# Kernel optimization log

Hardware: AMD Instinct MI355X
Metric: run time of the kernel (lower is better)

Reference implementation:

```python
import jax, jax.numpy as jnp
import numpy as np

B, N, E, P, PH, H = 4, 512, 768, 64, 32, 8
D = E // H  # 96
FFN = 3072

def _ln(x, g, b, eps=1e-5):
    mu = jnp.mean(x, axis=-1, keepdims=True)
    var = jnp.mean((x - mu) ** 2, axis=-1, keepdims=True)
    return (x - mu) * jax.lax.rsqrt(var + eps) * g + b

def setup_inputs() -> dict:
    key = jax.random.key(0)
    ks = iter(jax.random.split(key, 80))
    def f(*s):
        return jax.random.normal(next(ks), s, jnp.float32) * 0.02
    ones = lambda *s: jnp.ones(s, jnp.float32)
    zeros = lambda *s: jnp.zeros(s, jnp.float32)
    return {
        'x': jax.random.normal(next(ks), (B, N, E), jnp.float32),
        'pair': jax.random.normal(next(ks), (B, N, N, P), jnp.float32) * 0.5,
        'attn_mask': zeros(B, 1, N, N),
        'op_mask': ones(B, N, 1),
        'op_norm': ones(1) / N,
        'nlist': jax.random.randint(next(ks), (B, N, 64), 0, N),
        'wq': f(E, E), 'wk': f(E, E), 'wv': f(E, E),
        'wg': f(E, E), 'bg': zeros(E),
        'wo': f(E, E), 'bo': zeros(E),
        'ln_pair_g': ones(P), 'ln_pair_b': zeros(P),
        'wb': f(H, P), 'bb': zeros(H),
        'ln_attn_g': ones(E), 'ln_attn_b': zeros(E),
        'ln_ffn_g': ones(E), 'ln_ffn_b': zeros(E),
        'w_ffn1': f(FFN, E), 'b_ffn1': zeros(FFN),
        'w_ffn2': f(E, FFN), 'b_ffn2': zeros(E),
        'ln_opm_g': ones(E), 'ln_opm_b': zeros(E),
        'w_opm_in': f(2 * PH, E), 'b_opm_in': zeros(2 * PH),
        'w_opm_out': f(P, PH * PH), 'b_opm_out': zeros(P),
        'ln_tm_g': ones(P), 'ln_tm_b': zeros(P),
        'w_tm_abp': f(2 * PH, P), 'b_tm_abp': zeros(2 * PH),
        'w_tm_abg': f(2 * PH, P), 'b_tm_abg': zeros(2 * PH),
        'w_tm_g': f(P, P), 'b_tm_g': zeros(P),
        'w_tm_z': f(P, PH), 'b_tm_z': zeros(P),
        'ln_tmo_g': ones(PH), 'ln_tmo_b': zeros(PH),
        'ln_pffn_g': ones(P), 'ln_pffn_b': zeros(P),
        'w_pffn1': f(P, P), 'b_pffn1': zeros(P),
        'w_pffn2': f(P, P), 'b_pffn2': zeros(P),
    }

def _forward(x, pair, attn_mask, op_mask, op_norm, wq, wk, wv, wg, bg, wo, bo,
             ln_pair_g, ln_pair_b, wb, bb, ln_attn_g, ln_attn_b,
             ln_ffn_g, ln_ffn_b, w_ffn1, b_ffn1, w_ffn2, b_ffn2,
             ln_opm_g, ln_opm_b, w_opm_in, b_opm_in, w_opm_out, b_opm_out,
             ln_tm_g, ln_tm_b, w_tm_abp, b_tm_abp, w_tm_abg, b_tm_abg,
             w_tm_g, b_tm_g, w_tm_z, b_tm_z, ln_tmo_g, ln_tmo_b,
             ln_pffn_g, ln_pffn_b, w_pffn1, b_pffn1, w_pffn2, b_pffn2):
    Bx, Nx, _ = x.shape
    # --- gated pair-bias self-attention (pre-LN, eval mode: dropout = identity) ---
    h = _ln(x, ln_attn_g, ln_attn_b)
    pn = _ln(pair, ln_pair_g, ln_pair_b)               # AtomAttention pair LayerNorm
    bias = jnp.einsum('bijp,hp->bhij', pn, wb) + bb[None, :, None, None]
    q = (h @ wq.T).reshape(Bx, Nx, H, D).transpose(0, 2, 1, 3) * (D ** -0.5)
    k = (h @ wk.T).reshape(Bx, Nx, H, D).transpose(0, 2, 1, 3)
    v = (h @ wv.T).reshape(Bx, Nx, H, D).transpose(0, 2, 1, 3)
    attn = jax.nn.softmax(jnp.einsum('bhid,bhjd->bhij', q, k) + attn_mask + bias, axis=-1)
    o = jnp.einsum('bhij,bhjd->bhid', attn, v).transpose(0, 2, 1, 3).reshape(Bx, Nx, E)
    o = jax.nn.sigmoid(h @ wg.T + bg) * o              # sigmoid output gate
    x = x + (o @ wo.T + bo)
    # --- atom transition MLP ---
    h = _ln(x, ln_ffn_g, ln_ffn_b)
    x = x + (jax.nn.gelu(h @ w_ffn1.T + b_ffn1, approximate=False) @ w_ffn2.T + b_ffn2)
    # --- OuterProduct pair update (fused: avoids [B,N,N,PH*PH] intermediate) ---
    h = _ln(x, ln_opm_g, ln_opm_b)
    ab = (h @ w_opm_in.T + b_opm_in) * op_mask
    a_o, b_o = jnp.split(ab, 2, axis=-1)               # each [B,N,PH]
    z = jnp.einsum('bid,bje,pde->bijp', a_o, b_o, w_opm_out.reshape(P, PH, PH)) + b_opm_out
    pair = pair + z * op_norm
    # --- triangle multiplication ---
    zp = _ln(pair, ln_tm_g, ln_tm_b)
    gpr = zp @ w_tm_g.T + b_tm_g                       # gate (no sigmoid, matches source)
    ab = (zp @ w_tm_abp.T + b_tm_abp) * jax.nn.sigmoid(zp @ w_tm_abg.T + b_tm_abg)
    a_t, b_t = jnp.split(ab, 2, axis=-1)               # each [B,N,N,PH]
    t = jnp.einsum('bijh,bkjh->bhik', a_t, b_t) + jnp.einsum('bjih,bjkh->bhik', a_t, b_t)
    t = _ln(t.transpose(0, 2, 3, 1), ln_tmo_g, ln_tmo_b) @ w_tm_z.T + b_tm_z
    pair = pair + gpr * t
    # --- pair transition MLP ---
    zp = _ln(pair, ln_pffn_g, ln_pffn_b)
    pair = pair + (jax.nn.gelu(zp @ w_pffn1.T + b_pffn1, approximate=False) @ w_pffn2.T + b_pffn2)
    return x, pair

def reference(x, pair, attn_mask, op_mask, op_norm, nlist, wq, wk, wv, wg, bg, wo, bo,
              ln_pair_g, ln_pair_b, wb, bb, ln_attn_g, ln_attn_b,
              ln_ffn_g, ln_ffn_b, w_ffn1, b_ffn1, w_ffn2, b_ffn2,
              ln_opm_g, ln_opm_b, w_opm_in, b_opm_in, w_opm_out, b_opm_out,
              ln_tm_g, ln_tm_b, w_tm_abp, b_tm_abp, w_tm_abg, b_tm_abg,
              w_tm_g, b_tm_g, w_tm_z, b_tm_z, ln_tmo_g, ln_tmo_b,
              ln_pffn_g, ln_pffn_b, w_pffn1, b_pffn1, w_pffn2, b_pffn2):
    del nlist  # accepted by the torch module but unused in the math
    return _forward(x, pair, attn_mask, op_mask, op_norm, wq, wk, wv, wg, bg, wo, bo,
                    ln_pair_g, ln_pair_b, wb, bb, ln_attn_g, ln_attn_b,
                    ln_ffn_g, ln_ffn_b, w_ffn1, b_ffn1, w_ffn2, b_ffn2,
                    ln_opm_g, ln_opm_b, w_opm_in, b_opm_in, w_opm_out, b_opm_out,
                    ln_tm_g, ln_tm_b, w_tm_abp, b_tm_abp, w_tm_abg, b_tm_abg,
                    w_tm_g, b_tm_g, w_tm_z, b_tm_z, ln_tmo_g, ln_tmo_b,
                    ln_pffn_g, ln_pffn_b, w_pffn1, b_pffn1, w_pffn2, b_pffn2)
```

## Files before the change

### kernel.cpp

```cpp
#include <hip/hip_runtime.h>
#include <hip/hip_bf16.h>
#include <math.h>

#define Nn 512
#define Ee 768
#define Pp 64
#define PHh 32
#define Hh 8
#define Dd 96
#define NNe 262144
#define LNEPS 1e-5f

typedef __attribute__((ext_vector_type(8))) short bf8;
typedef __attribute__((ext_vector_type(4))) short bf4;
typedef __attribute__((ext_vector_type(4))) float f32x4;
#define MFMA(a,b,c) __builtin_amdgcn_mfma_f32_16x16x32_bf16(a,b,c,0,0,0)

__device__ __forceinline__ short f2bf(float f) {
  unsigned u = __builtin_bit_cast(unsigned, f);
  unsigned r = (u + 0x7fffu + ((u >> 16) & 1u)) >> 16;
  return (short)r;
}
__device__ __forceinline__ float bf2f(short s) {
  unsigned u = ((unsigned)(unsigned short)s) << 16;
// ... 244 lines not shown
        *(const bf8*)(A + (long)(m0 + r4 + 64) * 768 + k0 + c8);
    *(bf8*)&Bs[r4 * 40 + c8] = *(const bf8*)(W + (long)(n0 + r4) * 768 + k0 + c8);
    *(bf8*)&Bs[(r4 + 64) * 40 + c8] =
        *(const bf8*)(W + (long)(n0 + r4 + 64) * 768 + k0 + c8);
    __syncthreads();
    bf8 af[4], bfm[4];
#pragma unroll
    for (int mi = 0; mi < 4; ++mi)
      af[mi] = *(const bf8*)&As[(wr * 64 + mi * 16 + llo) * 40 + lhi * 8];
#pragma unroll
    for (int ni = 0; ni < 4; ++ni)
      bfm[ni] = *(const bf8*)&Bs[(wc * 64 + ni * 16 + llo) * 40 + lhi * 8];
#pragma unroll
    for (int mi = 0; mi < 4; ++mi)
#pragma unroll
      for (int ni = 0; ni < 4; ++ni)
        acc[mi][ni] = MFMA(af[mi], bfm[ni], acc[mi][ni]);
    __syncthreads();
  }
#pragma unroll
  for (int mi = 0; mi < 4; ++mi) {
    int gmb = m0 + wr * 64 + mi * 16 + lhi * 4;
#pragma unroll
    for (int ni = 0; ni < 4; ++ni) {
      int gn = n0 + wc * 64 + ni * 16 + llo;
      float bv = bias[gn];
#pragma unroll
      for (int r = 0; r < 4; ++r)
        outB[(long)(gmb + r) * 3072 + gn] = f2bf(gelu_exact(acc[mi][ni][r] + bv));
    }
  }
}

__global__ __launch_bounds__(256) void attn_fused(
    const short* __restrict__ q_bf, const short* __restrict__ k_bf,
    const short* __restrict__ bias_bf, const float* __restrict__ mask,
    short* __restrict__ out_bf) {
  int it = blockIdx.x, h = blockIdx.y, b = blockIdx.z;
  int tid = threadIdx.x;
  int wv = tid >> 6, lane = tid & 63;
  int lhi = lane >> 4, llo = lane & 15;
  int i0 = it * 16;
  long qoff = ((long)(b * 512 + i0)) * 768 + h * 96;
  bf8 qf[3];
#pragma unroll
  for (int ks = 0; ks < 3; ++ks)
    qf[ks] = *(const bf8*)(q_bf + qoff + (long)llo * 768 + ks * 32 + lhi * 8);
  long koff = ((long)b * 512) * 768 + h * 96;
  long bioff = (long)(b * 8 + h) * NNe + (long)i0 * 512;
  long moff = (long)b * NNe + (long)i0 * 512;
  float sv[8][4];
  int jb0 = wv * 128;
#pragma unroll
  for (int jf = 0; jf < 8; ++jf) {
    int jb = jb0 + jf * 16;
    f32x4 acc = {0.f, 0.f, 0.f, 0.f};
#pragma unroll
    for (int ks = 0; ks < 3; ++ks) {
      bf8 kf = *(const bf8*)(k_bf + koff + (long)(jb + llo) * 768 + ks * 32 + lhi * 8);
      acc = MFMA(qf[ks], kf, acc);
    }
#pragma unroll
    for (int r = 0; r < 4; ++r) {
      int irow = lhi * 4 + r;
      int j = jb + llo;
      float bia = bf2f(bias_bf[bioff + (long)irow * 512 + j]);
// ... 116 lines not shown
    }
    *(bf4*)&Zb[e * 72 + q * 16 + k * 4] = pk;
  }
  __syncthreads();
  int wv = tid >> 6, lane = tid & 63;
  int lhi = lane >> 4, llo = lane & 15;
  int n0 = wv * 16;
  f32x4 acc = {0.f, 0.f, 0.f, 0.f};
#pragma unroll
  for (int ks = 0; ks < 2; ++ks) {
    bf8 a = *(const bf8*)&Wb[llo * 72 + ks * 32 + lhi * 8];
    bf8 bz = *(const bf8*)&Zb[(n0 + llo) * 72 + ks * 32 + lhi * 8];
    acc = MFMA(a, bz, acc);
  }
  int elem = n0 + llo;
#pragma unroll
  for (int r = 0; r < 4; ++r) {
    int h = lhi * 4 + r;
    if (h < 8) bias[(long)(b * 8 + h) * NNe + ein + elem] = f2bf(acc[r] + bbv[h]);
  }
}

__global__ __launch_bounds__(256) void opm_ab_fused(
    const float* __restrict__ pair_in, const short* __restrict__ Tb,
    const short* __restrict__ bo_bf, const float* __restrict__ b_out,
    const float* __restrict__ op_norm, const float* __restrict__ gam,
    const float* __restrict__ bet, const short* __restrict__ wp_a,
    const float* __restrict__ b_abp, const short* __restrict__ wg_a,
    const float* __restrict__ b_abg,
    short* __restrict__ aN, short* __restrict__ bN) {
  int jt = blockIdx.x;
  int i = blockIdx.y;
  int tid = threadIdx.x;
  __shared__ __align__(16) short Tsb[64 * 40];
  __shared__ __align__(16) short Bob[64 * 40];
  __shared__ __align__(16) short Zb[64 * 72];
  __shared__ __align__(16) short Wp[64 * 72];
  __shared__ __align__(16) short Wg[64 * 72];
  __shared__ float spS[64][9];
  __shared__ float spQ[64][9];
  int wv = tid >> 6, lane = tid & 63;
  int wr = wv >> 1, wc = wv & 1;
  int lhi = lane >> 4, llo = lane & 15;
  int chb = wr * 32 + lhi * 4;
  {
    int p = tid >> 2, e8 = (tid & 3) * 8;
    *(bf8*)&Tsb[p * 40 + e8] = *(const bf8*)(Tb + (long)i * 2048 + p * 32 + e8);
    *(bf8*)&Bob[p * 40 + e8] = *(const bf8*)(bo_bf + (long)(jt * 64 + p) * 32 + e8);
  }
  for (int l = tid; l < 512; l += 256) {
    int r = l >> 3, c8 = (l & 7) * 8;
    *(bf8*)&Wp[r * 72 + c8] = *(const bf8*)(wp_a + r * 64 + c8);
    *(bf8*)&Wg[r * 72 + c8] = *(const bf8*)(wg_a + r * 64 + c8);
  }
  long ebase = (long)i * 512 + jt * 64;
  const float* pbase = pair_in + ebase * 64;
  f32x4 x[2][2];
#pragma unroll
  for (int mi = 0; mi < 2; ++mi)
#pragma unroll
    for (int ni = 0; ni < 2; ++ni)
      x[mi][ni] = *(const f32x4*)(pbase + (long)(wc * 32 + ni * 16 + llo) * 64 +
                                  chb + mi * 16);
  __syncthreads();
  f32x4 acc[2][2] = {};
  {
    bf8 a0 = *(const bf8*)&Tsb[(wr * 32 + llo) * 40 + lhi * 8];
    bf8 a1 = *(const bf8*)&Tsb[(wr * 32 + 16 + llo) * 40 + lhi * 8];
    bf8 b0 = *(const bf8*)&Bob[(wc * 32 + llo) * 40 + lhi * 8];
    bf8 b1 = *(const bf8*)&Bob[(wc * 32 + 16 + llo) * 40 + lhi * 8];
    acc[0][0] = MFMA(a0, b0, acc[0][0]);
    acc[0][1] = MFMA(a0, b1, acc[0][1]);
    acc[1][0] = MFMA(a1, b0, acc[1][0]);
    acc[1][1] = MFMA(a1, b1, acc[1][1]);
  }
  float nrm = op_norm[0];
#pragma unroll
  for (int mi = 0; mi < 2; ++mi) {
    f32x4 bo4 = *(const f32x4*)(b_out + chb + mi * 16);
#pragma unroll
    for (int ni = 0; ni < 2; ++ni)
#pragma unroll
      for (int r = 0; r < 4; ++r)
        x[mi][ni][r] += (acc[mi][ni][r] + bo4[r]) * nrm;
  }
#pragma unroll
  for (int ni = 0; ni < 2; ++ni) {
    float s = 0.f, ss = 0.f;
#pragma unroll
    for (int mi = 0; mi < 2; ++mi)
#pragma unroll
      for (int r = 0; r < 4; ++r) { float v = x[mi][ni][r]; s += v; ss += v * v; }
    int e = wc * 32 + ni * 16 + llo;
    spS[e][wr * 4 + lhi] = s;
    spQ[e][wr * 4 + lhi] = ss;
  }
  __syncthreads();
  float mu1[2], rs1[2];
#pragma unroll
  for (int ni = 0; ni < 2; ++ni) {
    int e = wc * 32 + ni * 16 + llo;
    float s = 0.f, q2 = 0.f;
#pragma unroll
    for (int k = 0; k < 8; ++k) { s += spS[e][k]; q2 += spQ[e][k]; }
    float mu = s * 0.015625f, var = q2 * 0.015625f - mu * mu;
    mu1[ni] = mu; rs1[ni] = rsqrtf(var + LNEPS);
  }
#pragma unroll
  for (int mi = 0; mi < 2; ++mi) {
    f32x4 gv = *(const f32x4*)(gam + chb + mi * 16);
    f32x4 bv = *(const f32x4*)(bet + chb + mi * 16);
#pragma unroll
    for (int ni = 0; ni < 2; ++ni) {
      int e = wc * 32 + ni * 16 + llo;
      bf4 pk;
#pragma unroll
      for (int r = 0; r < 4; ++r)
        pk[r] = f2bf((x[mi][ni][r] - mu1[ni]) * rs1[ni] * gv[r] + bv[r]);
      *(bf4*)&Zb[e * 72 + chb + mi * 16] = pk;
    }
  }
  __syncthreads();
  f32x4 ap[2][2] = {};
  f32x4 ag[2][2] = {};
#pragma unroll
  for (int ks = 0; ks < 2; ++ks) {
    bf8 z0 = *(const bf8*)&Zb[(wr * 32 + llo) * 72 + ks * 32 + lhi * 8];
    bf8 z1 = *(const bf8*)&Zb[(wr * 32 + 16 + llo) * 72 + ks * 32 + lhi * 8];
    bf8 p0 = *(const bf8*)&Wp[(wc * 32 + llo) * 72 + ks * 32 + lhi * 8];
    bf8 p1 = *(const bf8*)&Wp[(wc * 32 + 16 + llo) * 72 + ks * 32 + lhi * 8];
    bf8 g0 = *(const bf8*)&Wg[(wc * 32 + llo) * 72 + ks * 32 + lhi * 8];
    bf8 g1 = *(const bf8*)&Wg[(wc * 32 + 16 + llo) * 72 + ks * 32 + lhi * 8];
    ap[0][0] = MFMA(z0, p0, ap[0][0]);
    ap[0][1] = MFMA(z0, p1, ap[0][1]);
    ap[1][0] = MFMA(z1, p0, ap[1][0]);
    ap[1][1] = MFMA(z1, p1, ap[1][1]);
    ag[0][0] = MFMA(z0, g0, ag[0][0]);
    ag[0][1] = MFMA(z0, g1, ag[0][1]);
    ag[1][0] = MFMA(z1, g0, ag[1][0]);
    ag[1][1] = MFMA(z1, g1, ag[1][1]);
  }
#pragma unroll
  for (int mi = 0; mi < 2; ++mi) {
    int elemb = wr * 32 + mi * 16 + lhi * 4;
#pragma unroll
    for (int ni = 0; ni < 2; ++ni) {
      int ch = wc * 32 + ni * 16 + llo;
      float bp = b_abp[ch], bg = b_abg[ch];
      bf4 pack;
#pragma unroll
      for (int r = 0; r < 4; ++r)
        pack[r] = f2bf((ap[mi][ni][r] + bp) * sigmoidf_(ag[mi][ni][r] + bg));
      short* dst = (ch < 32) ? (aN + (long)ch * NNe) : (bN + (long)(ch - 32) * NNe);
      *(bf4*)(dst + ebase + elemb) = pack;
    }
  }
}

__global__ __launch_bounds__(512) void tm_tri_mfma(const short* __restrict__ aN,
                                                   const short* __restrict__ bN,
                                                   short* __restrict__ t_out) {
  int lin = blockIdx.z * 16 + blockIdx.y * 4 + blockIdx.x;
  int vid = (lin & 7) * 64 + (lin >> 3);
  int h = vid >> 4;
  int rem = vid & 15;
// ... 45 lines not shown
      bf8 c = *(const bf8*)&A2[(wr * 64 + mi * 16 + llo) * 40 + lhi * 8];
      acc[mi][0] = MFMA(c, dfr[0], acc[mi][0]);
      acc[mi][1] = MFMA(c, dfr[1], acc[mi][1]);
    }
    __syncthreads();
  }
  short* tp = t_out + (long)h * NNe;
#pragma unroll
  for (int mi = 0; mi < 4; ++mi)
#pragma unroll
    for (int ni = 0; ni < 2; ++ni) {
      int row = i0 + wr * 64 + mi * 16 + lhi * 4;
      int col = k0 + wc * 32 + ni * 16 + llo;
#pragma unroll
      for (int r = 0; r < 4; ++r) tp[(long)(row + r) * 512 + col] = f2bf(acc[mi][ni][r]);
    }
}

__global__ __launch_bounds__(256) void upd_pffn_fused(
    const float* __restrict__ pin, float* __restrict__ pout,
    const short* __restrict__ t_in,
    const short* __restrict__ Tb, const short* __restrict__ bo_bf,
    const float* __restrict__ b_out, const float* __restrict__ op_norm,
    const float* __restrict__ g_tm, const float* __restrict__ b_tm,
    const short* __restrict__ wg_a, const float* __restrict__ b_g,
    const short* __restrict__ wz_a, const float* __restrict__ b_z,
    const float* __restrict__ g_tmo, const float* __restrict__ b_tmo,
    const float* __restrict__ g_pf, const float* __restrict__ b_pf,
    const short* __restrict__ w1_a, const float* __restrict__ b1,
    const short* __restrict__ w2_a, const float* __restrict__ b2) {
  __shared__ __align__(16) short Zb[64 * 72];
  __shared__ __align__(16) short Tlb[64 * 40];
  __shared__ __align__(16) short Wbuf[64 * 72];
  __shared__ __align__(16) short Wzb[64 * 40];
  __shared__ __align__(16) short Tsb[64 * 40];
  __shared__ __align__(16) short Bob[64 * 40];
  __shared__ float spS[64][9];
  __shared__ float spQ[64][9];
  __shared__ float spB[4][2][72];
  int tid = threadIdx.x;
  long e0 = (long)blockIdx.x * 64;
  int i = (int)(e0 >> 9);
  int jt = (int)((e0 >> 6) & 7);
  int wv = tid >> 6, lane = tid & 63;
  int wr = wv >> 1, wc = wv & 1;
  int lhi = lane >> 4, llo = lane & 15;
  int chb = wr * 32 + lhi * 4;
  int r0 = tid >> 3, c0 = (tid & 7) * 8;
  int r1 = (tid + 256) >> 3, c1 = ((tid + 256) & 7) * 8;
  bf8 w1r0, w1r1, w2r0, w2r1;
  {
    *(bf8*)&Wbuf[r0 * 72 + c0] = *(const bf8*)(wg_a + r0 * 64 + c0);
    *(bf8*)&Wbuf[r1 * 72 + c1] = *(const bf8*)(wg_a + r1 * 64 + c1);
    w1r0 = *(const bf8*)(w1_a + r0 * 64 + c0);
    w1r1 = *(const bf8*)(w1_a + r1 * 64 + c1);
    w2r0 = *(const bf8*)(w2_a + r0 * 64 + c0);
    w2r1 = *(const bf8*)(w2_a + r1 * 64 + c1);
    int rz = tid >> 2, cz = (tid & 3) * 8;
    *(bf8*)&Wzb[rz * 40 + cz] = *(const bf8*)(wz_a + rz * 32 + cz);
    int p = tid >> 2, e8 = (tid & 3) * 8;
    *(bf8*)&Tsb[p * 40 + e8] = *(const bf8*)(Tb + (long)i * 2048 + p * 32 + e8);
    *(bf8*)&Bob[p * 40 + e8] = *(const bf8*)(bo_bf + (long)(jt * 64 + p) * 32 + e8);
  }
  f32x4 x[2][2];
#pragma unroll
  for (int mi = 0; mi < 2; ++mi)
#pragma unroll
    for (int ni = 0; ni < 2; ++ni)
      x[mi][ni] = *(const f32x4*)(pin + (e0 + wc * 32 + ni * 16 + llo) * 64 +
                                  chb + mi * 16);
  int te = tid & 63, tq = tid >> 6;
  float tt[8];
  {
    float sB = 0.f, ssB = 0.f;
#pragma unroll
    for (int k = 0; k < 8; ++k) {
      float v = bf2f(t_in[(long)(tq * 8 + k) * NNe + e0 + te]);
      tt[k] = v; sB += v; ssB += v * v;
    }
    spB[tq][0][te] = sB; spB[tq][1][te] = ssB;
  }
  __syncthreads();
  {
    float ts = spB[0][0][te] + spB[1][0][te] + spB[2][0][te] + spB[3][0][te];
    float tss = spB[0][1][te] + spB[1][1][te] + spB[2][1][te] + spB[3][1][te];
    float mu = ts * 0.03125f, var = tss * 0.03125f - mu * mu;
    float rs = rsqrtf(var + LNEPS);
    bf8 pk;
#pragma unroll
    for (int k = 0; k < 8; ++k) {
      int c = tq * 8 + k;
      pk[k] = f2bf((tt[k] - mu) * rs * g_tmo[c] + b_tmo[c]);
    }
    *(bf8*)&Tlb[te * 40 + tq * 8] = pk;
  }
  {
    f32x4 acc[2][2] = {};
    bf8 a0 = *(const bf8*)&Tsb[(wr * 32 + llo) * 40 + lhi * 8];
    bf8 a1 = *(const bf8*)&Tsb[(wr * 32 + 16 + llo) * 40 + lhi * 8];
    bf8 b0 = *(const bf8*)&Bob[(wc * 32 + llo) * 40 + lhi * 8];
    bf8 b1 = *(const bf8*)&Bob[(wc * 32 + 16 + llo) * 40 + lhi * 8];
    acc[0][0] = MFMA(a0, b0, acc[0][0]);
    acc[0][1] = MFMA(a0, b1, acc[0][1]);
    acc[1][0] = MFMA(a1, b0, acc[1][0]);
    acc[1][1] = MFMA(a1, b1, acc[1][1]);
    float nrm = op_norm[0];
#pragma unroll
    for (int mi = 0; mi < 2; ++mi) {
      f32x4 bo4 = *(const f32x4*)(b_out + chb + mi * 16);
#pragma unroll
      for (int ni = 0; ni < 2; ++ni)
#pragma unroll
        for (int r = 0; r < 4; ++r)
          x[mi][ni][r] += (acc[mi][ni][r] + bo4[r]) * nrm;
    }
  }
#pragma unroll
  for (int ni = 0; ni < 2; ++ni) {
    float s = 0.f, ss = 0.f;
#pragma unroll
    for (int mi = 0; mi < 2; ++mi)
#pragma unroll
      for (int r = 0; r < 4; ++r) { float v = x[mi][ni][r]; s += v; ss += v * v; }
    int e = wc * 32 + ni * 16 + llo;
    spS[e][wr * 4 + lhi] = s;
    spQ[e][wr * 4 + lhi] = ss;
  }
  __syncthreads();
  float mu1[2], rs1[2];
#pragma unroll
  for (int ni = 0; ni < 2; ++ni) {
    int e = wc * 32 + ni * 16 + llo;
    float s = 0.f, q2 = 0.f;
#pragma unroll
    for (int k = 0; k < 8; ++k) { s += spS[e][k]; q2 += spQ[e][k]; }
    float mu = s * 0.015625f, var = q2 * 0.015625f - mu * mu;
    mu1[ni] = mu; rs1[ni] = rsqrtf(var + LNEPS);
  }
#pragma unroll
  for (int mi = 0; mi < 2; ++mi) {
    f32x4 gv = *(const f32x4*)(g_tm + chb + mi * 16);
    f32x4 bv = *(const f32x4*)(b_tm + chb + mi * 16);
#pragma unroll
    for (int ni = 0; ni < 2; ++ni) {
      int e = wc * 32 + ni * 16 + llo;
      bf4 pk;
#pragma unroll
      for (int r = 0; r < 4; ++r)
        pk[r] = f2bf((x[mi][ni][r] - mu1[ni]) * rs1[ni] * gv[r] + bv[r]);
      *(bf4*)&Zb[e * 72 + chb + mi * 16] = pk;
    }
  }
  __syncthreads();
  f32x4 accg[2][2] = {};
  f32x4 accz[2][2] = {};
#pragma unroll
  for (int ks = 0; ks < 2; ++ks) {
    bf8 a0 = *(const bf8*)&Wbuf[(wr * 32 + llo) * 72 + ks * 32 + lhi * 8];
    bf8 a1 = *(const bf8*)&Wbuf[(wr * 32 + 16 + llo) * 72 + ks * 32 + lhi * 8];
    bf8 z0 = *(const bf8*)&Zb[(wc * 32 + llo) * 72 + ks * 32 + lhi * 8];
    bf8 z1 = *(const bf8*)&Zb[(wc * 32 + 16 + llo) * 72 + ks * 32 + lhi * 8];
    accg[0][0] = MFMA(a0, z0, accg[0][0]);
    accg[0][1] = MFMA(a0, z1, accg[0][1]);
    accg[1][0] = MFMA(a1, z0, accg[1][0]);
    accg[1][1] = MFMA(a1, z1, accg[1][1]);
  }
  {
    bf8 a0 = *(const bf8*)&Wzb[(wr * 32 + llo) * 40 + lhi * 8];
    bf8 a1 = *(const bf8*)&Wzb[(wr * 32 + 16 + llo) * 40 + lhi * 8];
    bf8 t0 = *(const bf8*)&Tlb[(wc * 32 + llo) * 40 + lhi * 8];
    bf8 t1 = *(const bf8*)&Tlb[(wc * 32 + 16 + llo) * 40 + lhi * 8];
    accz[0][0] = MFMA(a0, t0, accz[0][0]);
    accz[0][1] = MFMA(a0, t1, accz[0][1]);
    accz[1][0] = MFMA(a1, t0, accz[1][0]);
    accz[1][1] = MFMA(a1, t1, accz[1][1]);
  }
#pragma unroll
  for (int mi = 0; mi < 2; ++mi) {
    f32x4 bgv = *(const f32x4*)(b_g + chb + mi * 16);
    f32x4 bzv = *(const f32x4*)(b_z + chb + mi * 16);
#pragma unroll
    for (int ni = 0; ni < 2; ++ni)
#pragma unroll
      for (int r = 0; r < 4; ++r)
        x[mi][ni][r] += (accg[mi][ni][r] + bgv[r]) * (accz[mi][ni][r] + bzv[r]);
  }
#pragma unroll
  for (int ni = 0; ni < 2; ++ni) {
    float s = 0.f, ss = 0.f;
#pragma unroll
    for (int mi = 0; mi < 2; ++mi)
#pragma unroll
      for (int r = 0; r < 4; ++r) { float v = x[mi][ni][r]; s += v; ss += v * v; }
    int e = wc * 32 + ni * 16 + llo;
    spS[e][wr * 4 + lhi] = s;
    spQ[e][wr * 4 + lhi] = ss;
  }
  __syncthreads();
  *(bf8*)&Wbuf[r0 * 72 + c0] = w1r0;
  *(bf8*)&Wbuf[r1 * 72 + c1] = w1r1;
#pragma unroll
  for (int ni = 0; ni < 2; ++ni) {
    int e = wc * 32 + ni * 16 + llo;
    float s = 0.f, q2 = 0.f;
#pragma unroll
    for (int k = 0; k < 8; ++k) { s += spS[e][k]; q2 += spQ[e][k]; }
    float mu = s * 0.015625f, var = q2 * 0.015625f - mu * mu;
    mu1[ni] = mu; rs1[ni] = rsqrtf(var + LNEPS);
  }
#pragma unroll
  for (int mi = 0; mi < 2; ++mi) {
    f32x4 gv = *(const f32x4*)(g_pf + chb + mi * 16);
    f32x4 bv = *(const f32x4*)(b_pf + chb + mi * 16);
#pragma unroll
    for (int ni = 0; ni < 2; ++ni) {
      int e = wc * 32 + ni * 16 + llo;
      bf4 pk;
#pragma unroll
      for (int r = 0; r < 4; ++r)
        pk[r] = f2bf((x[mi][ni][r] - mu1[ni]) * rs1[ni] * gv[r] + bv[r]);
      *(bf4*)&Zb[e * 72 + chb + mi * 16] = pk;
    }
  }
  __syncthreads();
  f32x4 acc1[2][2] = {};
#pragma unroll
  for (int ks = 0; ks < 2; ++ks) {
    bf8 a0 = *(const bf8*)&Wbuf[(wr * 32 + llo) * 72 + ks * 32 + lhi * 8];
    bf8 a1 = *(const bf8*)&Wbuf[(wr * 32 + 16 + llo) * 72 + ks * 32 + lhi * 8];
    bf8 z0 = *(const bf8*)&Zb[(wc * 32 + llo) * 72 + ks * 32 + lhi * 8];
    bf8 z1 = *(const bf8*)&Zb[(wc * 32 + 16 + llo) * 72 + ks * 32 + lhi * 8];
    acc1[0][0] = MFMA(a0, z0, acc1[0][0]);
    acc1[0][1] = MFMA(a0, z1, acc1[0][1]);
    acc1[1][0] = MFMA(a1, z0, acc1[1][0]);
    acc1[1][1] = MFMA(a1, z1, acc1[1][1]);
  }
  __syncthreads();
  *(bf8*)&Wbuf[r0 * 72 + c0] = w2r0;
  *(bf8*)&Wbuf[r1 * 72 + c1] = w2r1;
#pragma unroll
  for (int mi = 0; mi < 2; ++mi) {
    f32x4 bv = *(const f32x4*)(b1 + chb + mi * 16);
#pragma unroll
    for (int ni = 0; ni < 2; ++ni) {
      int e = wc * 32 + ni * 16 + llo;
      bf4 pk;
#pragma unroll
      for (int r = 0; r < 4; ++r) pk[r] = f2bf(gelu_exact(acc1[mi][ni][r] + bv[r]));
      *(bf4*)&Zb[e * 72 + chb + mi * 16] = pk;
    }
  }
  __syncthreads();
  f32x4 acc2[2][2] = {};
#pragma unroll
  for (int ks = 0; ks < 2; ++ks) {
    bf8 a0 = *(const bf8*)&Wbuf[(wr * 32 + llo) * 72 + ks * 32 + lhi * 8];
    bf8 a1 = *(const bf8*)&Wbuf[(wr * 32 + 16 + llo) * 72 + ks * 32 + lhi * 8];
    bf8 z0 = *(const bf8*)&Zb[(wc * 32 + llo) * 72 + ks * 32 + lhi * 8];
    bf8 z1 = *(const bf8*)&Zb[(wc * 32 + 16 + llo) * 72 + ks * 32 + lhi * 8];
    acc2[0][0] = MFMA(a0, z0, acc2[0][0]);
    acc2[0][1] = MFMA(a0, z1, acc2[0][1]);
    acc2[1][0] = MFMA(a1, z0, acc2[1][0]);
    acc2[1][1] = MFMA(a1, z1, acc2[1][1]);
  }
#pragma unroll
  for (int mi = 0; mi < 2; ++mi) {
    f32x4 bv = *(const f32x4*)(b2 + chb + mi * 16);
#pragma unroll
    for (int ni = 0; ni < 2; ++ni) {
#pragma unroll
      for (int r = 0; r < 4; ++r) x[mi][ni][r] += acc2[mi][ni][r] + bv[r];
      *(f32x4*)(pout + (e0 + wc * 32 + ni * 16 + llo) * 64 + chb + mi * 16) =
          x[mi][ni];
    }
  }
}

extern "C" void kernel_launch(void* const* d_in, const int* in_sizes, int n_in,
                              void* d_out, int out_size, void* d_ws, size_t ws_size,
                              hipStream_t stream) {
  const float* x = (const float*)d_in[0];
  const float* pair = (const float*)d_in[1];
  const float* attn_mask = (const float*)d_in[2];
  const float* op_mask = (const float*)d_in[3];
  const float* op_norm = (const float*)d_in[4];
  const float* wq = (const float*)d_in[6];
  const float* wk = (const float*)d_in[7];
  const float* wv_ = (const float*)d_in[8];
  const float* wg = (const float*)d_in[9];
  const float* bg = (const float*)d_in[10];
  const float* wo = (const float*)d_in[11];
  const float* bo = (const float*)d_in[12];
// ... 54 lines not shown
  short* k_bf = (short*)(ws + 5442816);
  short* vT_bf = (short*)(ws + 6229248);
  float* gb = ws + 7015680;
  short* gb_bf = (short*)(ws + 10161408);
  float* x1b = ws + 10947840;
  short* biasb_bf = (short*)(ws + 12520704);
  short* attn_bf = (short*)(ws + 16715008);
  short* mffn_bf = (short*)(ws + 20909312);
  float* abb = ws + 24055040;
  short* abb_bf = (short*)(ws + 24186112);
  short* Tb_bf = (short*)(ws + 24218880);
  short* aNb = (short*)(ws + 4656384);
  short* bNb = (short*)(ws + 8850688);
  short* t_bf = (short*)(ws + 13044992);

  float* xo = (float*)d_out;
  float* pair1 = xo + 1572864;

  const float qscale = 0.1020620726159658f;

  castw_kernel<<<30144, 256, 0, stream>>>(wq, wk, wv_, wg, wo, w_ffn1, w_ffn2, w_opm_in,
                                          wbf, qscale);
  castw2_kernel<<<90, 256, 0, stream>>>(wb, w_tm_abp, w_tm_abg, w_tm_g, w_tm_z,
                                        w_pffn1, w_pffn2, wb_a);
  ln_bf_kernel<<<2048, 256, 0, stream>>>(x, h_bf, ln_attn_g, ln_attn_b, 768);
  gemm_qkvg<<<dim3(24, 16, 1), 256, 0, stream>>>(h_bf, wq_bf, q_bf, k_bf, vT_bf, gb, bg);
  pair_bias_mfma<<<16384, 256, 0, stream>>>(pair, ln_pair_g, ln_pair_b, wb_a, bb, biasb_bf);
  attn_fused<<<dim3(32, 8, 4), 256, 0, stream>>>(q_bf, k_bf, biasb_bf, attn_mask, attn_bf);
  gemm_bf<<<dim3(2, 8, 32), 256, 0, stream>>>(attn_bf, 512, 2097152, 262144,
                                              vT_bf, 512, 393216, 49152,
                                              nullptr, 0, 393216, 96, gb_bf, 768,
                                              gb, 768, 393216, 96, nullptr,
                                              512, 96, 512, 2, 0, 8);
  gemm_bf<<<dim3(12, 32, 1), 256, 0, stream>>>(gb_bf, 768, 0, 0, wo_bf, 768, 0, 0,
                                               x1b, 768, 0, 0, nullptr, 0,
                                               x, 768, 0, 0, bo,
                                               2048, 768, 768, 0, 0, 1);
  ln_bf_kernel<<<2048, 256, 0, stream>>>(x1b, h_bf, ln_ffn_g, ln_ffn_b, 768);
  gemm_ffn1<<<dim3(24, 16, 1), 256, 0, stream>>>(h_bf, wf1_bf, mffn_bf, b_ffn1);
  gemm_bf<<<dim3(12, 32, 1), 256, 0, stream>>>(mffn_bf, 3072, 0, 0, wf2_bf, 3072, 0, 0,
                                               xo, 768, 0, 0, nullptr, 0,
                                               x1b, 768, 0, 0, b_ffn2,
                                               2048, 768, 3072, 0, 0, 1);
  ln_bf_kernel<<<2048, 256, 0, stream>>>(xo, h_bf, ln_opm_g, ln_opm_b, 768);
  gemm_bf<<<dim3(1, 32, 1), 256, 0, stream>>>(h_bf, 768, 0, 0, wop_bf, 768, 0, 0,
                                              abb, 64, 0, 0, nullptr, 0,
                                              nullptr, 0, 0, 0, b_opm_in,
                                              2048, 64, 768, 0, 0, 1);
  opmask_kernel<<<512, 256, 0, stream>>>(abb, op_mask, abb_bf);
  opm_T_kernel<<<dim3(256, 64, 1), dim3(32, 8, 1), 0, stream>>>(abb, w_opm_out, Tb_bf);
  for (int b = 0; b < 4; ++b) {
    const float* pin = pair + (long)b * NNe * 64;
    float* pbb = pair1 + (long)b * NNe * 64;
    opm_ab_fused<<<dim3(8, 512, 1), 256, 0, stream>>>(
        pin, Tb_bf + (long)b * 1048576, abb_bf + (long)b * 16384, b_opm_out, op_norm,
        ln_tm_g, ln_tm_b, wabp_a, b_tm_abp, wabg_a, b_tm_abg, aNb, bNb);
    tm_tri_mfma<<<dim3(4, 4, 32), 512, 0, stream>>>(aNb, bNb, t_bf);
    upd_pffn_fused<<<4096, 256, 0, stream>>>(
        pin, pbb, t_bf, Tb_bf + (long)b * 1048576, abb_bf + (long)b * 16384,
        b_opm_out, op_norm,
        ln_tm_g, ln_tm_b, wtg_a, b_tm_g, wtz_a, b_tm_z,
        ln_tmo_g, ln_tmo_b, ln_pffn_g, ln_pffn_b, wp1_a, b_pffn1, wp2_a, b_pffn2);
  }
}
```

Before: 907.0 us.

## Use 128x128 GEMM for out-proj/FFN2 and load OPM fragments directly from global

```diff
diff --git a/kernel.cpp b/kernel.cpp
--- a/kernel.cpp
+++ b/kernel.cpp
@@ -300,6 +300,56 @@
   }
 }
 
+__global__ __launch_bounds__(256) void gemm128(
+    const short* __restrict__ A, const short* __restrict__ W, int K,
+    const float* __restrict__ resid, const float* __restrict__ bias,
+    float* __restrict__ outF) {
+  __shared__ __align__(16) short As[128 * 40];
+  __shared__ __align__(16) short Bs[128 * 40];
+  int m0 = blockIdx.y * 128, n0 = blockIdx.x * 128;
+  int tid = threadIdx.x;
+  int wv = tid >> 6, lane = tid & 63;
+  int wr = wv >> 1, wc = wv & 1;
+  int lhi = lane >> 4, llo = lane & 15;
+  int r4 = tid >> 2, c8 = (tid & 3) * 8;
+  f32x4 acc[4][4] = {};
+  for (int k0 = 0; k0 < K; k0 += 32) {
+    *(bf8*)&As[r4 * 40 + c8] = *(const bf8*)(A + (long)(m0 + r4) * K + k0 + c8);
+    *(bf8*)&As[(r4 + 64) * 40 + c8] =
+        *(const bf8*)(A + (long)(m0 + r4 + 64) * K + k0 + c8);
+    *(bf8*)&Bs[r4 * 40 + c8] = *(const bf8*)(W + (long)(n0 + r4) * K + k0 + c8);
+    *(bf8*)&Bs[(r4 + 64) * 40 + c8] =
+        *(const bf8*)(W + (long)(n0 + r4 + 64) * K + k0 + c8);
+    __syncthreads();
+    bf8 af[4], bfm[4];
+#pragma unroll
+    for (int mi = 0; mi < 4; ++mi)
+      af[mi] = *(const bf8*)&As[(wr * 64 + mi * 16 + llo) * 40 + lhi * 8];
+#pragma unroll
+    for (int ni = 0; ni < 4; ++ni)
+      bfm[ni] = *(const bf8*)&Bs[(wc * 64 + ni * 16 + llo) * 40 + lhi * 8];
+#pragma unroll
+    for (int mi = 0; mi < 4; ++mi)
+#pragma unroll
+      for (int ni = 0; ni < 4; ++ni)
+        acc[mi][ni] = MFMA(af[mi], bfm[ni], acc[mi][ni]);
+    __syncthreads();
+  }
+#pragma unroll
+  for (int mi = 0; mi < 4; ++mi) {
+    int gmb = m0 + wr * 64 + mi * 16 + lhi * 4;
+#pragma unroll
+    for (int ni = 0; ni < 4; ++ni) {
+      int gn = n0 + wc * 64 + ni * 16 + llo;
+      float bv = bias[gn];
+#pragma unroll
+      for (int r = 0; r < 4; ++r)
+        outF[(long)(gmb + r) * 768 + gn] =
+            acc[mi][ni][r] + bv + resid[(long)(gmb + r) * 768 + gn];
+    }
+  }
+}
+
 __global__ __launch_bounds__(256) void attn_fused(
     const short* __restrict__ q_bf, const short* __restrict__ k_bf,
     const short* __restrict__ bias_bf, const float* __restrict__ mask,
@@ -482,8 +532,6 @@
   int jt = blockIdx.x;
   int i = blockIdx.y;
   int tid = threadIdx.x;
-  __shared__ __align__(16) short Tsb[64 * 40];
-  __shared__ __align__(16) short Bob[64 * 40];
   __shared__ __align__(16) short Zb[64 * 72];
   __shared__ __align__(16) short Wp[64 * 72];
   __shared__ __align__(16) short Wg[64 * 72];
@@ -493,11 +541,7 @@
   int wr = wv >> 1, wc = wv & 1;
   int lhi = lane >> 4, llo = lane & 15;
   int chb = wr * 32 + lhi * 4;
-  {
-    int p = tid >> 2, e8 = (tid & 3) * 8;
-    *(bf8*)&Tsb[p * 40 + e8] = *(const bf8*)(Tb + (long)i * 2048 + p * 32 + e8);
-    *(bf8*)&Bob[p * 40 + e8] = *(const bf8*)(bo_bf + (long)(jt * 64 + p) * 32 + e8);
-  }
+  int fc = lhi * 8;
   for (int l = tid; l < 512; l += 256) {
     int r = l >> 3, c8 = (l & 7) * 8;
     *(bf8*)&Wp[r * 72 + c8] = *(const bf8*)(wp_a + r * 64 + c8);
@@ -512,27 +556,26 @@
     for (int ni = 0; ni < 2; ++ni)
       x[mi][ni] = *(const f32x4*)(pbase + (long)(wc * 32 + ni * 16 + llo) * 64 +
                                   chb + mi * 16);
-  __syncthreads();
-  f32x4 acc[2][2] = {};
   {
-    bf8 a0 = *(const bf8*)&Tsb[(wr * 32 + llo) * 40 + lhi * 8];
-    bf8 a1 = *(const bf8*)&Tsb[(wr * 32 + 16 + llo) * 40 + lhi * 8];
-    bf8 b0 = *(const bf8*)&Bob[(wc * 32 + llo) * 40 + lhi * 8];
-    bf8 b1 = *(const bf8*)&Bob[(wc * 32 + 16 + llo) * 40 + lhi * 8];
+    f32x4 acc[2][2] = {};
+    bf8 a0 = *(const bf8*)(Tb + (long)i * 2048 + (long)(wr * 32 + llo) * 32 + fc);
+    bf8 a1 = *(const bf8*)(Tb + (long)i * 2048 + (long)(wr * 32 + 16 + llo) * 32 + fc);
+    bf8 b0 = *(const bf8*)(bo_bf + (long)(jt * 64 + wc * 32 + llo) * 32 + fc);
+    bf8 b1 = *(const bf8*)(bo_bf + (long)(jt * 64 + wc * 32 + 16 + llo) * 32 + fc);
     acc[0][0] = MFMA(a0, b0, acc[0][0]);
     acc[0][1] = MFMA(a0, b1, acc[0][1]);
     acc[1][0] = MFMA(a1, b0, acc[1][0]);
     acc[1][1] = MFMA(a1, b1, acc[1][1]);
-  }
-  float nrm = op_norm[0];
-#pragma unroll
-  for (int mi = 0; mi < 2; ++mi) {
-    f32x4 bo4 = *(const f32x4*)(b_out + chb + mi * 16);
-#pragma unroll
-    for (int ni = 0; ni < 2; ++ni)
-#pragma unroll
-      for (int r = 0; r < 4; ++r)
-        x[mi][ni][r] += (acc[mi][ni][r] + bo4[r]) * nrm;
+    float nrm = op_norm[0];
+#pragma unroll
+    for (int mi = 0; mi < 2; ++mi) {
+      f32x4 bo4 = *(const f32x4*)(b_out + chb + mi * 16);
+#pragma unroll
+      for (int ni = 0; ni < 2; ++ni)
+#pragma unroll
+        for (int r = 0; r < 4; ++r)
+          x[mi][ni][r] += (acc[mi][ni][r] + bo4[r]) * nrm;
+    }
   }
 #pragma unroll
   for (int ni = 0; ni < 2; ++ni) {
@@ -575,12 +618,12 @@
   f32x4 ag[2][2] = {};
 #pragma unroll
   for (int ks = 0; ks < 2; ++ks) {
-    bf8 z0 = *(const bf8*)&Zb[(wr * 32 + llo) * 72 + ks * 32 + lhi * 8];
-    bf8 z1 = *(const bf8*)&Zb[(wr * 32 + 16 + llo) * 72 + ks * 32 + lhi * 8];
-    bf8 p0 = *(const bf8*)&Wp[(wc * 32 + llo) * 72 + ks * 32 + lhi * 8];
-    bf8 p1 = *(const bf8*)&Wp[(wc * 32 + 16 + llo) * 72 + ks * 32 + lhi * 8];
-    bf8 g0 = *(const bf8*)&Wg[(wc * 32 + llo) * 72 + ks * 32 + lhi * 8];
-    bf8 g1 = *(const bf8*)&Wg[(wc * 32 + 16 + llo) * 72 + ks * 32 + lhi * 8];
+    bf8 z0 = *(const bf8*)&Zb[(wr * 32 + llo) * 72 + ks * 32 + fc];
+    bf8 z1 = *(const bf8*)&Zb[(wr * 32 + 16 + llo) * 72 + ks * 32 + fc];
+    bf8 p0 = *(const bf8*)&Wp[(wc * 32 + llo) * 72 + ks * 32 + fc];
+    bf8 p1 = *(const bf8*)&Wp[(wc * 32 + 16 + llo) * 72 + ks * 32 + fc];
+    bf8 g0 = *(const bf8*)&Wg[(wc * 32 + llo) * 72 + ks * 32 + fc];
+    bf8 g1 = *(const bf8*)&Wg[(wc * 32 + 16 + llo) * 72 + ks * 32 + fc];
     ap[0][0] = MFMA(z0, p0, ap[0][0]);
     ap[0][1] = MFMA(z0, p1, ap[0][1]);
     ap[1][0] = MFMA(z1, p0, ap[1][0]);
@@ -692,20 +735,21 @@
   __shared__ __align__(16) short Zb[64 * 72];
   __shared__ __align__(16) short Tlb[64 * 40];
   __shared__ __align__(16) short Wbuf[64 * 72];
-  __shared__ __align__(16) short Wzb[64 * 40];
-  __shared__ __align__(16) short Tsb[64 * 40];
-  __shared__ __align__(16) short Bob[64 * 40];
+  __shared__ __align__(16) short Wzb[64 * 36];
   __shared__ float spS[64][9];
   __shared__ float spQ[64][9];
   __shared__ float spB[4][2][72];
   int tid = threadIdx.x;
   long e0 = (long)blockIdx.x * 64;
-  int i = (int)(e0 >> 9);
+  long growT = e0 >> 9;
   int jt = (int)((e0 >> 6) & 7);
   int wv = tid >> 6, lane = tid & 63;
   int wr = wv >> 1, wc = wv & 1;
   int lhi = lane >> 4, llo = lane & 15;
   int chb = wr * 32 + lhi * 4;
+  int fc = lhi * 8;
+  int fr0 = wr * 32 + llo, fr1 = fr0 + 16;
+  int br0 = wc * 32 + llo, br1 = br0 + 16;
   int r0 = tid >> 3, c0 = (tid & 7) * 8;
   int r1 = (tid + 256) >> 3, c1 = ((tid + 256) & 7) * 8;
   bf8 w1r0, w1r1, w2r0, w2r1;
@@ -717,10 +761,7 @@
     w2r0 = *(const bf8*)(w2_a + r0 * 64 + c0);
     w2r1 = *(const bf8*)(w2_a + r1 * 64 + c1);
     int rz = tid >> 2, cz = (tid & 3) * 8;
-    *(bf8*)&Wzb[rz * 40 + cz] = *(const bf8*)(wz_a + rz * 32 + cz);
-    int p = tid >> 2, e8 = (tid & 3) * 8;
-    *(bf8*)&Tsb[p * 40 + e8] = *(const bf8*)(Tb + (long)i * 2048 + p * 32 + e8);
-    *(bf8*)&Bob[p * 40 + e8] = *(const bf8*)(bo_bf + (long)(jt * 64 + p) * 32 + e8);
+    *(bf8*)&Wzb[rz * 36 + cz] = *(const bf8*)(wz_a + rz * 32 + cz);
   }
   f32x4 x[2][2];
 #pragma unroll
@@ -729,6 +770,38 @@
     for (int ni = 0; ni < 2; ++ni)
       x[mi][ni] = *(const f32x4*)(pin + (e0 + wc * 32 + ni * 16 + llo) * 64 +
                                   chb + mi * 16);
+  {
+    f32x4 acc[2][2] = {};
+    bf8 a0 = *(const bf8*)(Tb + growT * 2048 + (long)fr0 * 32 + fc);
+    bf8 a1 = *(const bf8*)(Tb + growT * 2048 + (long)fr1 * 32 + fc);
+    bf8 b0 = *(const bf8*)(bo_bf + (long)(jt * 64 + br0) * 32 + fc);
+    bf8 b1 = *(const bf8*)(bo_bf + (long)(jt * 64 + br1) * 32 + fc);
+    acc[0][0] = MFMA(a0, b0, acc[0][0]);
+    acc[0][1] = MFMA(a0, b1, acc[0][1]);
+    acc[1][0] = MFMA(a1, b0, acc[1][0]);
+    acc[1][1] = MFMA(a1, b1, acc[1][1]);
+    float nrm = op_norm[0];
+#pragma unroll
+    for (int mi = 0; mi < 2; ++mi) {
+      f32x4 bo4 = *(const f32x4*)(b_out + chb + mi * 16);
+#pragma unroll
+      for (int ni = 0; ni < 2; ++ni)
+#pragma unroll
+        for (int r = 0; r < 4; ++r)
+          x[mi][ni][r] += (acc[mi][ni][r] + bo4[r]) * nrm;
+    }
+  }
+#pragma unroll
+  for (int ni = 0; ni < 2; ++ni) {
+    float s = 0.f, ss = 0.f;
+#pragma unroll
+    for (int mi = 0; mi < 2; ++mi)
+#pragma unroll
+      for (int r = 0; r < 4; ++r) { float v = x[mi][ni][r]; s += v; ss += v * v; }
+    int e = wc * 32 + ni * 16 + llo;
+    spS[e][wr * 4 + lhi] = s;
+    spQ[e][wr * 4 + lhi] = ss;
+  }
   int te = tid & 63, tq = tid >> 6;
   float tt[8];
   {
@@ -754,26 +827,63 @@
     }
     *(bf8*)&Tlb[te * 40 + tq * 8] = pk;
   }
+  float mu1[2], rs1[2];
+#pragma unroll
+  for (int ni = 0; ni < 2; ++ni) {
+    int e = wc * 32 + ni * 16 + llo;
+    float s = 0.f, q2 = 0.f;
+#pragma unroll
+    for (int k = 0; k < 8; ++k) { s += spS[e][k]; q2 += spQ[e][k]; }
+    float mu = s * 0.015625f, var = q2 * 0.015625f - mu * mu;
+    mu1[ni] = mu; rs1[ni] = rsqrtf(var + LNEPS);
+  }
+#pragma unroll
+  for (int mi = 0; mi < 2; ++mi) {
+    f32x4 gv = *(const f32x4*)(g_tm + chb + mi * 16);
+    f32x4 bv = *(const f32x4*)(b_tm + chb + mi * 16);
+#pragma unroll
+    for (int ni = 0; ni < 2; ++ni) {
+      int e = wc * 32 + ni * 16 + llo;
+      bf4 pk;
+#pragma unroll
+      for (int r = 0; r < 4; ++r)
+        pk[r] = f2bf((x[mi][ni][r] - mu1[ni]) * rs1[ni] * gv[r] + bv[r]);
+      *(bf4*)&Zb[e * 72 + chb + mi * 16] = pk;
+    }
+  }
+  __syncthreads();
+  f32x4 accg[2][2] = {};
+  f32x4 accz[2][2] = {};
+#pragma unroll
+  for (int ks = 0; ks < 2; ++ks) {
+    bf8 a0 = *(const bf8*)&Wbuf[fr0 * 72 + ks * 32 + fc];
+    bf8 a1 = *(const bf8*)&Wbuf[fr1 * 72 + ks * 32 + fc];
+    bf8 z0 = *(const bf8*)&Zb[br0 * 72 + ks * 32 + fc];
+    bf8 z1 = *(const bf8*)&Zb[br1 * 72 + ks * 32 + fc];
+    accg[0][0] = MFMA(a0, z0, accg[0][0]);
+    accg[0][1] = MFMA(a0, z1, accg[0][1]);
+    accg[1][0] = MFMA(a1, z0, accg[1][0]);
+    accg[1][1] = MFMA(a1, z1, accg[1][1]);
+  }
   {
-    f32x4 acc[2][2] = {};
-    bf8 a0 = *(const bf8*)&Tsb[(wr * 32 + llo) * 40 + lhi * 8];
-    bf8 a1 = *(const bf8*)&Tsb[(wr * 32 + 16 + llo) * 40 + lhi * 8];
-    bf8 b0 = *(const bf8*)&Bob[(wc * 32 + llo) * 40 + lhi * 8];
-    bf8 b1 = *(const bf8*)&Bob[(wc * 32 + 16 + llo) * 40 + lhi * 8];
-    acc[0][0] = MFMA(a0, b0, acc[0][0]);
-    acc[0][1] = MFMA(a0, b1, acc[0][1]);
-    acc[1][0] = MFMA(a1, b0, acc[1][0]);
-    acc[1][1] = MFMA(a1, b1, acc[1][1]);
-    float nrm = op_norm[0];
-#pragma unroll
-    for (int mi = 0; mi < 2; ++mi) {
-      f32x4 bo4 = *(const f32x4*)(b_out + chb + mi * 16);
-#pragma unroll
-      for (int ni = 0; ni < 2; ++ni)
-#pragma unroll
-        for (int r = 0; r < 4; ++r)
-          x[mi][ni][r] += (acc[mi][ni][r] + bo4[r]) * nrm;
-    }
+    bf8 a0 = *(const bf8*)&Wzb[fr0 * 36 + fc];
+    bf8 a1 = *(const bf8*)&Wzb[fr1 * 36 + fc];
+    bf8 t0 = *(const bf8*)&Tlb[br0 * 40 + fc];
+    bf8 t1 = *(const bf8*)&Tlb[br1 * 40 + fc];
+    accz[0][0] = MFMA(a0, t0, accz[0][0]);
+    accz[0][1] = MFMA(a0, t1, accz[0][1]);
+    accz[1][0] = MFMA(a1, t0, accz[1][0]);
+    accz[1][1] = MFMA(a1, t1, accz[1][1]);
+  }
+#pragma unroll
+  for (int mi = 0; mi < 2; ++mi) {
+    f32x4 bgv = *(const f32x4*)(b_g + chb + mi * 16);
+    f32x4 bzv = *(const f32x4*)(b_z + chb + mi * 16);
+#pragma unroll
+    for (int ni = 0; ni < 2; ++ni)
+#pragma unroll
+      for (int r = 0; r < 4; ++r)
+        x[mi][ni][r] += (accg[mi][ni][r] + bgv[r]) * (accz[mi][ni][r] + bzv[r]);
   }
 #pragma unroll
   for (int ni = 0; ni < 2; ++ni) {
@@ -787,7 +897,8 @@
     spQ[e][wr * 4 + lhi] = ss;
   }
   __syncthreads();
-  float mu1[2], rs1[2];
+  *(bf8*)&Wbuf[r0 * 72 + c0] = w1r0;
+  *(bf8*)&Wbuf[r1 * 72 + c1] = w1r1;
 #pragma unroll
   for (int ni = 0; ni < 2; ++ni) {
     int e = wc * 32 + ni * 16 + llo;
@@ -799,8 +910,8 @@
   }
 #pragma unroll
   for (int mi = 0; mi < 2; ++mi) {
-    f32x4 gv = *(const f32x4*)(g_tm + chb + mi * 16);
-    f32x4 bv = *(const f32x4*)(b_tm + chb + mi * 16);
+    f32x4 gv = *(const f32x4*)(g_pf + chb + mi * 16);
+    f32x4 bv = *(const f32x4*)(b_pf + chb + mi * 16);
 #pragma unroll
     for (int ni = 0; ni < 2; ++ni) {
       int e = wc * 32 + ni * 16 + llo;
@@ -812,84 +923,13 @@
     }
   }
   __syncthreads();
-  f32x4 accg[2][2] = {};
-  f32x4 accz[2][2] = {};
+  f32x4 acc1[2][2] = {};
 #pragma unroll
   for (int ks = 0; ks < 2; ++ks) {
-    bf8 a0 = *(const bf8*)&Wbuf[(wr * 32 + llo) * 72 + ks * 32 + lhi * 8];
-    bf8 a1 = *(const bf8*)&Wbuf[(wr * 32 + 16 + llo) * 72 + ks * 32 + lhi * 8];
-    bf8 z0 = *(const bf8*)&Zb[(wc * 32 + llo) * 72 + ks * 32 + lhi * 8];
-    bf8 z1 = *(const bf8*)&Zb[(wc * 32 + 16 + llo) * 72 + ks * 32 + lhi * 8];
-    accg[0][0] = MFMA(a0, z0, accg[0][0]);
-    accg[0][1] = MFMA(a0, z1, accg[0][1]);
-    accg[1][0] = MFMA(a1, z0, accg[1][0]);
-    accg[1][1] = MFMA(a1, z1, accg[1][1]);
-  }
-  {
-    bf8 a0 = *(const bf8*)&Wzb[(wr * 32 + llo) * 40 + lhi * 8];
-    bf8 a1 = *(const bf8*)&Wzb[(wr * 32 + 16 + llo) * 40 + lhi * 8];
-    bf8 t0 = *(const bf8*)&Tlb[(wc * 32 + llo) * 40 + lhi * 8];
-    bf8 t1 = *(const bf8*)&Tlb[(wc * 32 + 16 + llo) * 40 + lhi * 8];
-    accz[0][0] = MFMA(a0, t0, accz[0][0]);
-    accz[0][1] = MFMA(a0, t1, accz[0][1]);
-    accz[1][0] = MFMA(a1, t0, accz[1][0]);
-    accz[1][1] = MFMA(a1, t1, accz[1][1]);
-  }
-#pragma unroll
-  for (int mi = 0; mi < 2; ++mi) {
-    f32x4 bgv = *(const f32x4*)(b_g + chb + mi * 16);
-    f32x4 bzv = *(const f32x4*)(b_z + chb + mi * 16);
-#pragma unroll
-    for (int ni = 0; ni < 2; ++ni)
-#pragma unroll
-      for (int r = 0; r < 4; ++r)
-        x[mi][ni][r] += (accg[mi][ni][r] + bgv[r]) * (accz[mi][ni][r] + bzv[r]);
-  }
-#pragma unroll
-  for (int ni = 0; ni < 2; ++ni) {
-    float s = 0.f, ss = 0.f;
-#pragma unroll
-    for (int mi = 0; mi < 2; ++mi)
-#pragma unroll
-      for (int r = 0; r < 4; ++r) { float v = x[mi][ni][r]; s += v; ss += v * v; }
-    int e = wc * 32 + ni * 16 + llo;
-    spS[e][wr * 4 + lhi] = s;
-    spQ[e][wr * 4 + lhi] = ss;
-  }
-  __syncthreads();
-  *(bf8*)&Wbuf[r0 * 72 + c0] = w1r0;
-  *(bf8*)&Wbuf[r1 * 72 + c1] = w1r1;
-#pragma unroll
-  for (int ni = 0; ni < 2; ++ni) {
-    int e = wc * 32 + ni * 16 + llo;
-    float s = 0.f, q2 = 0.f;
-#pragma unroll
-    for (int k = 0; k < 8; ++k) { s += spS[e][k]; q2 += spQ[e][k]; }
-    float mu = s * 0.015625f, var = q2 * 0.015625f - mu * mu;
-    mu1[ni] = mu; rs1[ni] = rsqrtf(var + LNEPS);
-  }
-#pragma unroll
-  for (int mi = 0; mi < 2; ++mi) {
-    f32x4 gv = *(const f32x4*)(g_pf + chb + mi * 16);
-    f32x4 bv = *(const f32x4*)(b_pf + chb + mi * 16);
-#pragma unroll
-    for (int ni = 0; ni < 2; ++ni) {
-      int e = wc * 32 + ni * 16 + llo;
-      bf4 pk;
-#pragma unroll
-      for (int r = 0; r < 4; ++r)
-        pk[r] = f2bf((x[mi][ni][r] - mu1[ni]) * rs1[ni] * gv[r] + bv[r]);
-      *(bf4*)&Zb[e * 72 + chb + mi * 16] = pk;
-    }
-  }
-  __syncthreads();
-  f32x4 acc1[2][2] = {};
-#pragma unroll
-  for (int ks = 0; ks < 2; ++ks) {
-    bf8 a0 = *(const bf8*)&Wbuf[(wr * 32 + llo) * 72 + ks * 32 + lhi * 8];
-    bf8 a1 = *(const bf8*)&Wbuf[(wr * 32 + 16 + llo) * 72 + ks * 32 + lhi * 8];
-    bf8 z0 = *(const bf8*)&Zb[(wc * 32 + llo) * 72 + ks * 32 + lhi * 8];
-    bf8 z1 = *(const bf8*)&Zb[(wc * 32 + 16 + llo) * 72 + ks * 32 + lhi * 8];
+    bf8 a0 = *(const bf8*)&Wbuf[fr0 * 72 + ks * 32 + fc];
+    bf8 a1 = *(const bf8*)&Wbuf[fr1 * 72 + ks * 32 + fc];
+    bf8 z0 = *(const bf8*)&Zb[br0 * 72 + ks * 32 + fc];
+    bf8 z1 = *(const bf8*)&Zb[br1 * 72 + ks * 32 + fc];
     acc1[0][0] = MFMA(a0, z0, acc1[0][0]);
     acc1[0][1] = MFMA(a0, z1, acc1[0][1]);
     acc1[1][0] = MFMA(a1, z0, acc1[1][0]);
@@ -914,10 +954,10 @@
   f32x4 acc2[2][2] = {};
 #pragma unroll
   for (int ks = 0; ks < 2; ++ks) {
-    bf8 a0 = *(const bf8*)&Wbuf[(wr * 32 + llo) * 72 + ks * 32 + lhi * 8];
-    bf8 a1 = *(const bf8*)&Wbuf[(wr * 32 + 16 + llo) * 72 + ks * 32 + lhi * 8];
-    bf8 z0 = *(const bf8*)&Zb[(wc * 32 + llo) * 72 + ks * 32 + lhi * 8];
-    bf8 z1 = *(const bf8*)&Zb[(wc * 32 + 16 + llo) * 72 + ks * 32 + lhi * 8];
+    bf8 a0 = *(const bf8*)&Wbuf[fr0 * 72 + ks * 32 + fc];
+    bf8 a1 = *(const bf8*)&Wbuf[fr1 * 72 + ks * 32 + fc];
+    bf8 z0 = *(const bf8*)&Zb[br0 * 72 + ks * 32 + fc];
+    bf8 z1 = *(const bf8*)&Zb[br1 * 72 + ks * 32 + fc];
     acc2[0][0] = MFMA(a0, z0, acc2[0][0]);
     acc2[0][1] = MFMA(a0, z1, acc2[0][1]);
     acc2[1][0] = MFMA(a1, z0, acc2[1][0]);
@@ -1038,16 +1078,10 @@
                                               nullptr, 0, 393216, 96, gb_bf, 768,
                                               gb, 768, 393216, 96, nullptr,
                                               512, 96, 512, 2, 0, 8);
-  gemm_bf<<<dim3(12, 32, 1), 256, 0, stream>>>(gb_bf, 768, 0, 0, wo_bf, 768, 0, 0,
-                                               x1b, 768, 0, 0, nullptr, 0,
-                                               x, 768, 0, 0, bo,
-                                               2048, 768, 768, 0, 0, 1);
+  gemm128<<<dim3(6, 16, 1), 256, 0, stream>>>(gb_bf, wo_bf, 768, x, bo, x1b);
   ln_bf_kernel<<<2048, 256, 0, stream>>>(x1b, h_bf, ln_ffn_g, ln_ffn_b, 768);
   gemm_ffn1<<<dim3(24, 16, 1), 256, 0, stream>>>(h_bf, wf1_bf, mffn_bf, b_ffn1);
-  gemm_bf<<<dim3(12, 32, 1), 256, 0, stream>>>(mffn_bf, 3072, 0, 0, wf2_bf, 3072, 0, 0,
-                                               xo, 768, 0, 0, nullptr, 0,
-                                               x1b, 768, 0, 0, b_ffn2,
-                                               2048, 768, 3072, 0, 0, 1);
+  gemm128<<<dim3(6, 16, 1), 256, 0, stream>>>(mffn_bf, wf2_bf, 3072, x1b, b_ffn2, xo);
   ln_bf_kernel<<<2048, 256, 0, stream>>>(xo, h_bf, ln_opm_g, ln_opm_b, 768);
   gemm_bf<<<dim3(1, 32, 1), 256, 0, stream>>>(h_bf, 768, 0, 0, wop_bf, 768, 0, 0,
                                               abb, 64, 0, 0, nullptr, 0,
```

Result: no change. 916.8 us (+1.1%).
